# Kernel optimization log

Hardware: AMD Instinct MI355X
Metric: run time of the kernel (lower is better)

The kernel has to match this reference:

```python
import jax, jax.numpy as jnp
import numpy as np

N_HEADS = 16
DIM = 1024
BS, SLEN = 2, 2048
EPS = 1e-12  # F.normalize eps


def setup_inputs() -> dict:
    key = jax.random.key(0)
    ks = jax.random.split(key, 10)
    d = DIM
    inp = {
        "x": jax.random.normal(ks[0], (BS, SLEN, d), dtype=jnp.float32),
        # causal attention mask, as produced by get_masks(causal=True)
        "mask": jnp.tril(jnp.ones((SLEN, SLEN), dtype=bool))[None].repeat(BS, axis=0),
        "Wq": jax.random.normal(ks[1], (d, d), dtype=jnp.float32) / np.sqrt(d),
        "bq": jax.random.normal(ks[2], (d,), dtype=jnp.float32) * 0.02,
        "Wk": jax.random.normal(ks[3], (d, d), dtype=jnp.float32) / np.sqrt(d),
        "bk": jax.random.normal(ks[4], (d,), dtype=jnp.float32) * 0.02,
        "Wv": jax.random.normal(ks[5], (d, d), dtype=jnp.float32) / np.sqrt(d),
        "bv": jax.random.normal(ks[6], (d,), dtype=jnp.float32) * 0.02,
        "Wo": jax.random.normal(ks[7], (d, d), dtype=jnp.float32) / np.sqrt(d),
        "bo": jax.random.normal(ks[8], (d,), dtype=jnp.float32) * 0.02,
        # learnable scale for normalized (cosine) attention
        "attention_scale": jnp.ones((1,), dtype=jnp.float32) / np.sqrt(d // N_HEADS),
    }
    return inp


def _shape(t, bs, h, dph):
    # (bs, len, dim) -> (bs, h, len, dph)
    return t.reshape(bs, -1, h, dph).transpose(0, 2, 1, 3)


def reference(x, mask, Wq, bq, Wk, bk, Wv, bv, Wo, bo, attention_scale):
    bs, qlen, dim = x.shape
    h = N_HEADS
    dph = dim // h

    q = _shape(x @ Wq + bq, bs, h, dph)  # (bs, h, qlen, dph)
    k = _shape(x @ Wk + bk, bs, h, dph)
    v = _shape(x @ Wv + bv, bs, h, dph)

    # normalized (cosine) attention: L2-normalize q and k, learned scale
    q = q / jnp.maximum(jnp.linalg.norm(q, axis=-1, keepdims=True), EPS)
    k = k / jnp.maximum(jnp.linalg.norm(k, axis=-1, keepdims=True), EPS)
    q = q * attention_scale

    scores = jnp.einsum("bhqd,bhkd->bhqk", q, k)  # (bs, h, qlen, klen)
    scores = jnp.where(mask[:, None, :, :], scores, -jnp.inf)
    weights = jax.nn.softmax(scores, axis=-1)

    ctx = jnp.einsum("bhqk,bhkd->bhqd", weights, v)
    ctx = ctx.transpose(0, 2, 1, 3).reshape(bs, qlen, dim)
    return ctx @ Wo + bo
```

## Files before the change

### kernel.cpp

```cpp
#include <hip/hip_runtime.h>
#include <math.h>

#define NH 16
#define DPH 64
#define SLEN 2048
#define BSZ 2
#define DIM 1024
#define NTOK (BSZ * SLEN)
#define LOG2E 1.44269504088896f

typedef unsigned short ushortT;
typedef __attribute__((ext_vector_type(8))) short short8;
typedef __attribute__((ext_vector_type(4))) short s16x4;
typedef __attribute__((ext_vector_type(4))) float f32x4;

typedef __attribute__((address_space(1))) const unsigned int gu32c;
typedef __attribute__((address_space(3))) unsigned int lu32;

__device__ __forceinline__ void gld16(const void* g, void* l) {
    __builtin_amdgcn_global_load_lds((gu32c*)g, (lu32*)l, 16, 0, 0);
}

__device__ __forceinline__ ushortT f2bf(float f) {
    unsigned int u = __builtin_bit_cast(unsigned int, f);
    u = u + 0x7fffu + ((u >> 16) & 1u);
    return (ushortT)(u >> 16);
}

__global__ __launch_bounds__(256) void cvt_x(const float* __restrict__ x,
                                             ushortT* __restrict__ xb) {
    size_t i = (size_t)blockIdx.x * 256 + threadIdx.x;
    float4 a = *(const float4*)&x[i * 8];
    float4 b = *(const float4*)&x[i * 8 + 4];
    short8 v;
    v[0] = (short)f2bf(a.x); v[1] = (short)f2bf(a.y);
    v[2] = (short)f2bf(a.z); v[3] = (short)f2bf(a.w);
    v[4] = (short)f2bf(b.x); v[5] = (short)f2bf(b.y);
    v[6] = (short)f2bf(b.z); v[7] = (short)f2bf(b.w);
    *(short8*)&xb[i * 8] = v;
}

__global__ __launch_bounds__(256) void cvt_wt(const float* __restrict__ W0, const float* __restrict__ W1,
                                              const float* __restrict__ W2, const float* __restrict__ W3,
                                              ushortT* __restrict__ T0, ushortT* __restrict__ T1,
                                              ushortT* __restrict__ T2, ushortT* __restrict__ T3) {
    const float* W = blockIdx.z == 0 ? W0 : blockIdx.z == 1 ? W1 : blockIdx.z == 2 ? W2 : W3;
    ushortT* T = blockIdx.z == 0 ? T0 : blockIdx.z == 1 ? T1 : blockIdx.z == 2 ? T2 : T3;
    __shared__ float tile[64][65];
    const int tid = threadIdx.x;
    const int kb = blockIdx.y * 64, nb = blockIdx.x * 64;
#pragma unroll
    for (int it = 0; it < 4; it++) {
        int chunk = it * 256 + tid;
        int r = chunk >> 4, c4 = (chunk & 15) * 4;
        *(float4*)&tile[r][c4] = *(const float4*)&W[(size_t)(kb + r) * DIM + nb + c4];
    }
    __syncthreads();
#pragma unroll
    for (int it = 0; it < 2; it++) {
        int chunk = it * 256 + tid;
        int n = chunk >> 3, k8 = (chunk & 7) * 8;
        short8 o;
#pragma unroll
        for (int j = 0; j < 8; j++) o[j] = (short)f2bf(tile[k8 + j][n]);
        *(short8*)&T[(size_t)(nb + n) * DIM + kb + k8] = o;
    }
}

__device__ __forceinline__ void stage_tile(const ushortT* __restrict__ A,
                                           const ushortT* __restrict__ Bt,
                                           ushortT* lds, int row0, int col0,
                                           int kc, int bb, int srow, int sphys) {
#pragma unroll
    for (int h = 0; h < 4; h++) {
        int rl = (h & 1) * 128 + srow;
        int lch = sphys ^ (((rl >> 3) & 1) << 1);
        const ushortT* g = (h < 2) ? &A[(size_t)(row0 + rl) * DIM + kc + lch * 8]
                                   : &Bt[(size_t)(col0 + rl) * DIM + kc + lch * 8];
        int lb = ((h < 2) ? 0 : 32768) + bb * 16384 + rl * 32 + sphys * 8;
        gld16(g, &lds[lb]);
        gld16(g + 32, &lds[lb + 8192]);
    }
}

__global__ __launch_bounds__(512, 2) void gemm_qkv8(const ushortT* __restrict__ A,
                                                    const ushortT* __restrict__ Bt,
                                                    const float* __restrict__ bq,
                                                    const float* __restrict__ bk,
                                                    const float* __restrict__ bv,
                                                    const float* __restrict__ ascale,
                                                    ushortT* __restrict__ Qb,
                                                    ushortT* __restrict__ Kb,
                                                    ushortT* __restrict__ VF) {
    __shared__ __align__(16) ushortT lds[65536];
    const int tid = threadIdx.x;
    const int lane = tid & 63, wid = tid >> 6;
    const int wm = wid >> 2, wn = wid & 3;
    const int lo = lane & 15, hi = lane >> 4;
    const int bid = blockIdx.x;
    const int swz = (bid & 7) * 24 + (bid >> 3);
    const int bx = swz % 12, by = swz / 12;
    const int row0 = by * 256, col0 = bx * 256;
    const int srow = tid >> 2, sphys = tid & 3;
    f32x4 acc[8][4] = {};

    stage_tile(A, Bt, lds, row0, col0, 0, 0, srow, sphys);

    for (int tt = 0; tt < 16; ++tt) {
        const int bb = tt & 1;
        const int abase = bb * 16384, bbase = 32768 + bb * 16384;
#pragma unroll
        for (int ph = 0; ph < 4; ++ph) {
            const int ks = ph & 1, mh = ph >> 1;
            if (ph == 0) {
                asm volatile("s_waitcnt vmcnt(0)" ::: "memory");
                asm volatile("s_barrier" ::: "memory");
            }
            short8 af[4], bfr[4];
#pragma unroll
            for (int mm = 0; mm < 4; mm++) {
                int row = wm * 128 + (mh * 4 + mm) * 16 + lo;
                int phys = hi ^ (((row >> 3) & 1) << 1);
                af[mm] = *(const short8*)&lds[abase + ks * 8192 + row * 32 + phys * 8];
            }
#pragma unroll
            for (int n = 0; n < 4; n++) {
                int row = wn * 64 + n * 16 + lo;
                int phys = hi ^ (((row >> 3) & 1) << 1);
                bfr[n] = *(const short8*)&lds[bbase + ks * 8192 + row * 32 + phys * 8];
            }
            if (ph == 0 && tt < 15)
                stage_tile(A, Bt, lds, row0, col0, (tt + 1) * 64, bb ^ 1, srow, sphys);
            __builtin_amdgcn_s_setprio(1);
#pragma unroll
            for (int mm = 0; mm < 4; mm++)
#pragma unroll
                for (int n = 0; n < 4; n++)
                    acc[mh * 4 + mm][n] = __builtin_amdgcn_mfma_f32_16x16x32_bf16(
                        af[mm], bfr[n], acc[mh * 4 + mm][n], 0, 0, 0);
            __builtin_amdgcn_s_setprio(0);
            asm volatile("s_barrier" ::: "memory");
        }
    }

    const int cg = col0 + wn * 64;
    const int which = cg >> 10;
    const int cwin = cg & 1023;
    const int h = cwin >> 6;
    const int t0g = row0 + wm * 128;
    const int b = t0g >> 11, tok0 = t0g & (SLEN - 1);
    const float* bias = which == 0 ? bq : which == 1 ? bk : bv;

    float bb4[4];
#pragma unroll
    for (int n = 0; n < 4; n++) bb4[n] = bias[cwin + n * 16 + lo];
#pragma unroll
    for (int m = 0; m < 8; m++)
#pragma unroll
        for (int n = 0; n < 4; n++)
#pragma unroll
            for (int r = 0; r < 4; r++) acc[m][n][r] += bb4[n];

    if (which < 2) {
        float asc = (which == 0) ? ascale[0] * LOG2E : 1.0f;
#pragma unroll
        for (int m = 0; m < 8; m++)
#pragma unroll
            for (int r = 0; r < 4; r++) {
                float ss = acc[m][0][r] * acc[m][0][r] + acc[m][1][r] * acc[m][1][r] +
                           acc[m][2][r] * acc[m][2][r] + acc[m][3][r] * acc[m][3][r];
#pragma unroll
                for (int o = 8; o > 0; o >>= 1) ss += __shfl_xor(ss, o);
                float sc = asc / fmaxf(sqrtf(ss), 1e-12f);
#pragma unroll
                for (int n = 0; n < 4; n++) acc[m][n][r] *= sc;
            }
    }

    ushortT* tl = &lds[wid * 8192];
    if (which < 2) {
#pragma unroll
        for (int m = 0; m < 8; m++)
#pragma unroll
            for (int n = 0; n < 4; n++)
#pragma unroll
                for (int r = 0; r < 4; r++) {
                    int row = m * 16 + 4 * hi + r;
                    int c = n * 2 + (lo >> 3);
                    tl[row * 64 + ((c ^ (row & 7)) << 3) + (lo & 7)] = f2bf(acc[m][n][r]);
                }
        ushortT* op = which == 0 ? Qb : Kb;
        const size_t base = ((size_t)(b * NH + h) * SLEN + tok0) * DPH;
#pragma unroll
        for (int j = 0; j < 16; j++) {
            int cid = j * 64 + lane;
            int rowL = cid >> 3, c = cid & 7;
            uint4 v = *(const uint4*)&tl[rowL * 64 + ((c ^ (rowL & 7)) << 3)];
            *(uint4*)&op[base + (size_t)cid * 8] = v;
        }
    } else {
#pragma unroll
        for (int m = 0; m < 8; m++)
#pragma unroll
            for (int n = 0; n < 4; n++)
#pragma unroll
                for (int r = 0; r < 4; r++) {
                    int row = m * 16 + 4 * hi + r;
                    int c = n * 2 + (lo >> 3);
                    tl[row * 64 + ((c ^ ((row >> 3) & 7)) << 3) + (lo & 7)] = f2bf(acc[m][n][r]);
                }
        const int bh = b * NH + h;
        const int kt0 = tok0 >> 6;
#pragma unroll
        for (int i = 0; i < 16; i++) {
            int kk = i >> 3;
            int c = i & 7;
            int jd = c >> 1, ks2 = c & 1;
            int colL = jd * 16 + lo;
            int c2 = colL >> 3;
            short8 v;
#pragma unroll
            for (int e = 0; e < 8; e++) {
                int rowL = kk * 64 + ks2 * 32 + 8 * hi + e;
                v[e] = (short)tl[rowL * 64 + ((c2 ^ ((rowL >> 3) & 7)) << 3) + (colL & 7)];
            }
            *(short8*)&VF[((size_t)bh * 32 + kt0 + kk) * 4096 + (size_t)(c * 64 + lane) * 8] = v;
        }
    }
}

__global__ __launch_bounds__(256) void gemm_oproj(const ushortT* __restrict__ A,
                                                  const ushortT* __restrict__ Bt,
                                                  const float* __restrict__ bias,
                                                  float* __restrict__ outF) {
    __shared__ __align__(16) unsigned char lbuf[32768];
    ushortT* As = (ushortT*)lbuf;
    ushortT* Bs = (ushortT*)(lbuf + 8192);
    const int tid = threadIdx.x;
    const int lane = tid & 63, wid = tid >> 6;
    const int wr = wid >> 1, wc = wid & 1;
    const int lo = lane & 15, hi = lane >> 4;
    const int row0 = blockIdx.y * 64, col0 = blockIdx.x * 128;
    const int r8 = lane >> 3, sp = lane & 7;
    const int srcoff = (sp ^ r8) << 3;
    f32x4 acc[2][4] = {};

    for (int kc = 0; kc < DIM; kc += 64) {
        __syncthreads();
#pragma unroll
        for (int it = 0; it < 2; it++) {
            int seg = it * 4 + wid;
            int row = seg * 8 + r8;
            gld16(&A[(size_t)(row0 + row) * DIM + kc + srcoff], &As[seg * 512]);
        }
#pragma unroll
        for (int it = 0; it < 4; it++) {
            int seg = it * 4 + wid;
            int row = seg * 8 + r8;
            gld16(&Bt[(size_t)(col0 + row) * DIM + kc + srcoff], &Bs[seg * 512]);
        }
        __syncthreads();
#pragma unroll
        for (int ks = 0; ks < 2; ks++) {
            short8 af[2], bfr[4];
#pragma unroll
            for (int m = 0; m < 2; m++) {
                int row = wr * 32 + m * 16 + lo;
                af[m] = *(const short8*)&As[row * 64 + (((ks * 4 + hi) ^ (row & 7)) << 3)];
            }
#pragma unroll
            for (int n = 0; n < 4; n++) {
                int row = wc * 64 + n * 16 + lo;
                bfr[n] = *(const short8*)&Bs[row * 64 + (((ks * 4 + hi) ^ (row & 7)) << 3)];
            }
#pragma unroll
            for (int m = 0; m < 2; m++)
#pragma unroll
                for (int n = 0; n < 4; n++)
                    acc[m][n] = __builtin_amdgcn_mfma_f32_16x16x32_bf16(af[m], bfr[n], acc[m][n], 0, 0, 0);
        }
    }

    float bb[4];
#pragma unroll
    for (int n = 0; n < 4; n++) bb[n] = bias[col0 + wc * 64 + n * 16 + lo];
#pragma unroll
    for (int m = 0; m < 2; m++)
#pragma unroll
        for (int n = 0; n < 4; n++)
#pragma unroll
            for (int r = 0; r < 4; r++) acc[m][n][r] += bb[n];

    __syncthreads();
    float* tl = (float*)(lbuf + wid * 8192);
#pragma unroll
    for (int m = 0; m < 2; m++)
#pragma unroll
        for (int n = 0; n < 4; n++)
#pragma unroll
            for (int r = 0; r < 4; r++) {
                int row = m * 16 + hi * 4 + r;
                int col = n * 16 + lo;
                int cc = col >> 2;
                tl[row * 64 + ((cc ^ (row & 7)) << 2) + (col & 3)] = acc[m][n][r];
            }
#pragma unroll
    for (int j = 0; j < 8; j++) {
        int cid = j * 64 + lane;
        int rowR = cid >> 4, cc = cid & 15;
        f32x4 v = *(const f32x4*)&tl[rowR * 64 + ((cc ^ (rowR & 7)) << 2)];
        int rg = row0 + wr * 32 + rowR;
        int cgl = col0 + wc * 64 + cc * 4;
        *(f32x4*)&outF[(size_t)rg * DIM + cgl] = v;
    }
}

__global__ __launch_bounds__(512, 4) void attn(const ushortT* __restrict__ Q,
                                               const ushortT* __restrict__ K,
                                               const ushortT* __restrict__ VF,
                                               const float* __restrict__ scale,
                                               ushortT* __restrict__ ctx) {
    __shared__ __align__(16) ushortT Ks[64 * 64];
    __shared__ __align__(16) ushortT Ps[8 * 16 * 64];
    const int tid = threadIdx.x, lane = tid & 63, wid = tid >> 6;
    const int wg = wid & 3, sg = wid >> 2;
    const int bh = blockIdx.x, p = blockIdx.y;
    const int qt = sg ? p : 31 - p;
    const int kbmax = 31 - p;
    const size_t hb = (size_t)bh * SLEN * DPH;
    const int lo = lane & 15, hi = lane >> 4;
    const float mshift = fabsf(scale[0]) * LOG2E;

    short8 aq[2];
    {
        const int qrow = qt * 64 + wg * 16 + lo;
#pragma unroll
        for (int ks = 0; ks < 2; ks++)
            aq[ks] = *(const short8*)&Q[hb + (size_t)qrow * DPH + ks * 32 + 8 * hi];
    }

    const int srow = tid >> 3, sslot = tid & 7;
    const int sldsoff = srow * 64 + ((sslot ^ (srow & 7)) << 3);
    uint4 kr = *(const uint4*)&K[hb + (size_t)srow * DPH + sslot * 8];
    *(uint4*)&Ks[sldsoff] = kr;
    __syncthreads();

    f32x4 accd[4] = {};
    float lp = 0.f;

    for (int kb = 0; kb <= kbmax; kb++) {
        if (kb < kbmax)
            kr = *(const uint4*)&K[hb + (size_t)((kb + 1) * 64 + srow) * DPH + sslot * 8];

        if (kb <= qt) {
            short8 bv[8];
            const ushortT* vt = &VF[(((size_t)bh * 32 + kb) * 512 + lane) * 8];
#pragma unroll
            for (int c = 0; c < 8; c++) bv[c] = *(const short8*)&vt[(size_t)c * 512];

            f32x4 sf[4] = {};
#pragma unroll
            for (int ks = 0; ks < 2; ks++)
#pragma unroll
                for (int j = 0; j < 4; j++) {
                    int row = j * 16 + lo;
                    short8 bk = *(const short8*)&Ks[row * 64 + (((ks * 4 + hi) ^ (row & 7)) << 3)];
                    sf[j] = __builtin_amdgcn_mfma_f32_16x16x32_bf16(bk, aq[ks], sf[j], 0, 0, 0);
                }

            if (kb == qt) {
#pragma unroll
                for (int j = 0; j < 4; j++)
#pragma unroll
                    for (int r = 0; r < 4; r++)
                        if (j * 16 + 4 * hi + r > wg * 16 + lo) sf[j][r] = -INFINITY;
            }

#pragma unroll
            for (int j = 0; j < 4; j++) {
                s16x4 pk;
#pragma unroll
                for (int r = 0; r < 4; r++) {
                    float pv = __builtin_amdgcn_exp2f(sf[j][r] - mshift);
                    lp += pv;
                    pk[r] = (short)f2bf(pv);
                }
                int slot = (4 * j + hi) ^ (2 * (lo & 7));
                *(s16x4*)&Ps[wid * 1024 + lo * 64 + slot * 4] = pk;
            }

#pragma unroll
            for (int ks = 0; ks < 2; ks++) {
                int slot0 = (8 * ks + 2 * hi) ^ (2 * (lo & 7));
                short8 ap = *(const short8*)&Ps[wid * 1024 + lo * 64 + slot0 * 4];
#pragma unroll
                for (int jd = 0; jd < 4; jd++)
                    accd[jd] = __builtin_amdgcn_mfma_f32_16x16x32_bf16(ap, bv[jd * 2 + ks], accd[jd], 0, 0, 0);
            }
        }

        __syncthreads();
        if (kb < kbmax) {
            *(uint4*)&Ks[sldsoff] = kr;
            __syncthreads();
        }
    }

    lp += __shfl_xor(lp, 16);
    lp += __shfl_xor(lp, 32);

    const int b = bh >> 4, h = bh & 15;
#pragma unroll
    for (int r = 0; r < 4; r++) {
        float lr = __shfl(lp, (lane & 48) | (4 * hi + r));
        float inv = 1.0f / lr;
        int t = qt * 64 + wg * 16 + 4 * hi + r;
#pragma unroll
        for (int jd = 0; jd < 4; jd++) {
            int d = jd * 16 + lo;
            ctx[(size_t)(b * SLEN + t) * DIM + h * 64 + d] = f2bf(accd[jd][r] * inv);
        }
    }
}

extern "C" void kernel_launch(void* const* d_in, const int* in_sizes, int n_in,
                              void* d_out, int out_size, void* d_ws,
                              size_t ws_size, hipStream_t stream) {
    const float* x = (const float*)d_in[0];
    const float* Wq = (const float*)d_in[2];
    const float* bq = (const float*)d_in[3];
    const float* Wk = (const float*)d_in[4];
    const float* bk = (const float*)d_in[5];
    const float* Wv = (const float*)d_in[6];
    const float* bv = (const float*)d_in[7];
    const float* Wo = (const float*)d_in[8];
    const float* bo = (const float*)d_in[9];
    const float* ascale = (const float*)d_in[10];
    float* outF = (float*)d_out;

    unsigned char* ws = (unsigned char*)d_ws;
    const size_t MB = 1u << 20;
    ushortT* xb = (ushortT*)(ws);
    ushortT* Wqkvt = (ushortT*)(ws + 8 * MB);
    ushortT* Wot = (ushortT*)(ws + 14 * MB);
    ushortT* Qb = (ushortT*)(ws + 16 * MB);
    ushortT* Kb = (ushortT*)(ws + 24 * MB);
    ushortT* VFb = (ushortT*)(ws + 32 * MB);
    ushortT* ctxb = (ushortT*)(ws + 40 * MB);

    cvt_x<<<NTOK * DIM / (8 * 256), 256, 0, stream>>>(x, xb);
    cvt_wt<<<dim3(16, 16, 4), 256, 0, stream>>>(Wq, Wk, Wv, Wo, Wqkvt,
                                                Wqkvt + (size_t)1024 * 1024,
                                                Wqkvt + (size_t)2048 * 1024, Wot);

    gemm_qkv8<<<dim3(192), 512, 0, stream>>>(xb, Wqkvt, bq, bk, bv, ascale, Qb, Kb, VFb);

    attn<<<dim3(32, 16), 512, 0, stream>>>(Qb, Kb, VFb, ascale, ctxb);

    gemm_oproj<<<dim3(DIM / 128, NTOK / 64), 256, 0, stream>>>(ctxb, Wot, bo, outF);
}
```

Before: 106.8 us.

## Pipeline QKV GEMM LDS staging at half-K-tile granularity with vmcnt-gated waits

```diff
diff --git a/kernel.cpp b/kernel.cpp
--- a/kernel.cpp
+++ b/kernel.cpp
@@ -64,22 +64,6 @@
 #pragma unroll
         for (int j = 0; j < 8; j++) o[j] = (short)f2bf(tile[k8 + j][n]);
         *(short8*)&T[(size_t)(nb + n) * DIM + kb + k8] = o;
-    }
-}
-
-__device__ __forceinline__ void stage_tile(const ushortT* __restrict__ A,
-                                           const ushortT* __restrict__ Bt,
-                                           ushortT* lds, int row0, int col0,
-                                           int kc, int bb, int srow, int sphys) {
-#pragma unroll
-    for (int h = 0; h < 4; h++) {
-        int rl = (h & 1) * 128 + srow;
-        int lch = sphys ^ (((rl >> 3) & 1) << 1);
-        const ushortT* g = (h < 2) ? &A[(size_t)(row0 + rl) * DIM + kc + lch * 8]
-                                   : &Bt[(size_t)(col0 + rl) * DIM + kc + lch * 8];
-        int lb = ((h < 2) ? 0 : 32768) + bb * 16384 + rl * 32 + sphys * 8;
-        gld16(g, &lds[lb]);
-        gld16(g + 32, &lds[lb + 8192]);
     }
 }
 
@@ -101,47 +85,97 @@
     const int swz = (bid & 7) * 24 + (bid >> 3);
     const int bx = swz % 12, by = swz / 12;
     const int row0 = by * 256, col0 = bx * 256;
-    const int srow = tid >> 2, sphys = tid & 3;
+    const int srow2 = tid >> 2, sc = tid & 3;
     f32x4 acc[8][4] = {};
-
-    stage_tile(A, Bt, lds, row0, col0, 0, 0, srow, sphys);
-
-    for (int tt = 0; tt < 16; ++tt) {
-        const int bb = tt & 1;
-        const int abase = bb * 16384, bbase = 32768 + bb * 16384;
-#pragma unroll
-        for (int ph = 0; ph < 4; ++ph) {
-            const int ks = ph & 1, mh = ph >> 1;
-            if (ph == 0) {
-                asm volatile("s_waitcnt vmcnt(0)" ::: "memory");
-                asm volatile("s_barrier" ::: "memory");
-            }
-            short8 af[4], bfr[4];
-#pragma unroll
-            for (int mm = 0; mm < 4; mm++) {
-                int row = wm * 128 + (mh * 4 + mm) * 16 + lo;
-                int phys = hi ^ (((row >> 3) & 1) << 1);
-                af[mm] = *(const short8*)&lds[abase + ks * 8192 + row * 32 + phys * 8];
-            }
-#pragma unroll
-            for (int n = 0; n < 4; n++) {
-                int row = wn * 64 + n * 16 + lo;
-                int phys = hi ^ (((row >> 3) & 1) << 1);
-                bfr[n] = *(const short8*)&lds[bbase + ks * 8192 + row * 32 + phys * 8];
-            }
-            if (ph == 0 && tt < 15)
-                stage_tile(A, Bt, lds, row0, col0, (tt + 1) * 64, bb ^ 1, srow, sphys);
-            __builtin_amdgcn_s_setprio(1);
-#pragma unroll
-            for (int mm = 0; mm < 4; mm++)
-#pragma unroll
-                for (int n = 0; n < 4; n++)
-                    acc[mh * 4 + mm][n] = __builtin_amdgcn_mfma_f32_16x16x32_bf16(
-                        af[mm], bfr[n], acc[mh * 4 + mm][n], 0, 0, 0);
-            __builtin_amdgcn_s_setprio(0);
-            asm volatile("s_barrier" ::: "memory");
-        }
-    }
+    short8 af[4], bfr[4];
+
+    auto stage = [&](int isA, int buf, int ksh, int kt) {
+        const ushortT* g = isA ? A : Bt;
+        int r0 = isA ? row0 : col0;
+        int base = (isA ? 0 : 32768) + (buf * 2 + ksh) * 8192;
+#pragma unroll
+        for (int r = 0; r < 2; r++) {
+            int rl = r * 128 + srow2;
+            int gch = sc ^ ((rl >> 1) & 3);
+            gld16(&g[(size_t)(r0 + rl) * DIM + kt * 64 + ksh * 32 + gch * 8],
+                  &lds[base + r * 4096 + tid * 8]);
+        }
+    };
+    auto loadA = [&](int buf, int ks, int mh) {
+        int base = (buf * 2 + ks) * 8192;
+#pragma unroll
+        for (int mm = 0; mm < 4; mm++) {
+            int row = wm * 128 + (mh * 4 + mm) * 16 + lo;
+            af[mm] = *(const short8*)&lds[base + row * 32 + (hi ^ ((row >> 1) & 3)) * 8];
+        }
+    };
+    auto loadB = [&](int buf, int ks) {
+        int base = 32768 + (buf * 2 + ks) * 8192;
+#pragma unroll
+        for (int n = 0; n < 4; n++) {
+            int row = wn * 64 + n * 16 + lo;
+            bfr[n] = *(const short8*)&lds[base + row * 32 + (hi ^ ((row >> 1) & 3)) * 8];
+        }
+    };
+    auto mfma16 = [&](int mh) {
+        __builtin_amdgcn_s_setprio(1);
+#pragma unroll
+        for (int mm = 0; mm < 4; mm++)
+#pragma unroll
+            for (int n = 0; n < 4; n++)
+                acc[mh * 4 + mm][n] = __builtin_amdgcn_mfma_f32_16x16x32_bf16(
+                    af[mm], bfr[n], acc[mh * 4 + mm][n], 0, 0, 0);
+        __builtin_amdgcn_s_setprio(0);
+    };
+
+    stage(1, 0, 0, 0); stage(0, 0, 0, 0);
+    stage(1, 0, 1, 0); stage(0, 0, 1, 0);
+    stage(1, 1, 0, 1); stage(0, 1, 0, 1);
+
+#pragma unroll 1
+    for (int it = 0; it < 8; ++it) {
+        const int o = it * 2 + 1;
+        const bool more = (it < 7);
+        asm volatile("s_waitcnt vmcnt(8)" ::: "memory");
+        asm volatile("s_barrier" ::: "memory");
+        loadA(0, 0, 0); loadB(0, 0);
+        stage(1, 1, 1, o);
+        mfma16(0);
+        asm volatile("s_barrier" ::: "memory");
+        loadA(0, 0, 1);
+        stage(0, 1, 1, o);
+        mfma16(1);
+        asm volatile("s_waitcnt vmcnt(8)" ::: "memory");
+        asm volatile("s_barrier" ::: "memory");
+        loadA(0, 1, 0); loadB(0, 1);
+        if (more) stage(1, 0, 0, o + 1);
+        mfma16(0);
+        asm volatile("s_barrier" ::: "memory");
+        loadA(0, 1, 1);
+        if (more) stage(0, 0, 0, o + 1);
+        mfma16(1);
+        if (more) { asm volatile("s_waitcnt vmcnt(8)" ::: "memory"); }
+        else      { asm volatile("s_waitcnt vmcnt(4)" ::: "memory"); }
+        asm volatile("s_barrier" ::: "memory");
+        loadA(1, 0, 0); loadB(1, 0);
+        if (more) stage(1, 0, 1, o + 1);
+        mfma16(0);
+        asm volatile("s_barrier" ::: "memory");
+        loadA(1, 0, 1);
+        if (more) stage(0, 0, 1, o + 1);
+        mfma16(1);
+        if (more) { asm volatile("s_waitcnt vmcnt(8)" ::: "memory"); }
+        else      { asm volatile("s_waitcnt vmcnt(0)" ::: "memory"); }
+        asm volatile("s_barrier" ::: "memory");
+        loadA(1, 1, 0); loadB(1, 1);
+        if (more) stage(1, 1, 0, o + 2);
+        mfma16(0);
+        asm volatile("s_barrier" ::: "memory");
+        loadA(1, 1, 1);
+        if (more) stage(0, 1, 0, o + 2);
+        mfma16(1);
+    }
+    __syncthreads();
 
     const int cg = col0 + wn * 64;
     const int which = cg >> 10;
@@ -171,9 +205,9 @@
                            acc[m][2][r] * acc[m][2][r] + acc[m][3][r] * acc[m][3][r];
 #pragma unroll
                 for (int o = 8; o > 0; o >>= 1) ss += __shfl_xor(ss, o);
-                float sc = asc / fmaxf(sqrtf(ss), 1e-12f);
-#pragma unroll
-                for (int n = 0; n < 4; n++) acc[m][n][r] *= sc;
+                float sc2 = asc / fmaxf(sqrtf(ss), 1e-12f);
+#pragma unroll
+                for (int n = 0; n < 4; n++) acc[m][n][r] *= sc2;
             }
     }
 
```

Result: faster. 102.3 us (-4.2%).
